# Kernel optimization log

Hardware: AMD Instinct MI355X
Metric: run time of the kernel (lower is better)

The kernel has to match this reference:

```python
import jax, jax.numpy as jnp
import numpy as np

N_NODES = 100000
N_EDGES = 500000
D = 128


def setup_inputs() -> dict:
    key = jax.random.key(0)
    ks = jax.random.split(key, 6)
    x = jax.random.normal(ks[0], (N_NODES, D), dtype=jnp.float32)
    edge_index = jax.random.randint(ks[1], (2, N_EDGES), 0, N_NODES, dtype=jnp.int64)
    edge_label = jax.random.randint(ks[2], (N_EDGES,), 0, 2, dtype=jnp.int64)
    # MLP params (dim_in -> dim_in, 2 layers, has_act=True, has_bias=True)
    scale = 1.0 / np.sqrt(D)
    W1 = jax.random.normal(ks[3], (D, D), dtype=jnp.float32) * scale
    b1 = jnp.zeros((D,), dtype=jnp.float32)
    W2 = jax.random.normal(ks[4], (D, D), dtype=jnp.float32) * scale
    b2 = jnp.zeros((D,), dtype=jnp.float32)
    return {"x": x, "edge_index": edge_index, "edge_label": edge_label,
            "W1": W1, "b1": b1, "W2": W2, "b2": b2}


def reference(x, edge_index, edge_label, W1, b1, W2, b2):
    # post-MP MLP on all node features (has_act=True -> ReLU after each layer)
    h = jax.nn.relu(x @ W1 + b1)          # [N, D]
    h = jax.nn.relu(h @ W2 + b2)          # [N, D]
    # gather endpoints: batch.x[edge_index] -> [2, E, D]
    v1 = h[edge_index[0]]                  # [E, D]
    v2 = h[edge_index[1]]                  # [E, D]
    # dot decode: sum(v1 * v2, dim=-1)
    pred = jnp.sum(v1 * v2, axis=-1)       # [E]
    return pred, edge_label
```

## Files before the change

### kernel.cpp

```cpp
#include <hip/hip_runtime.h>

typedef __attribute__((ext_vector_type(8))) short short8;
typedef __attribute__((ext_vector_type(4))) short short4v;
typedef __attribute__((ext_vector_type(4))) float floatx4;

#define D 128
#define NWAVES 4
#define GRID_MLP 512

__device__ __forceinline__ unsigned short f2bf(float f) {
  unsigned u = __float_as_uint(f);
  u += 0x7FFFu + ((u >> 16) & 1u);
  return (unsigned short)(u >> 16);
}

__device__ __forceinline__ void stageW(const float* __restrict__ W,
                                       unsigned short* __restrict__ sW, int tid) {
  const int n = tid & 127;
  const int tg = tid >> 7;
  #pragma unroll
  for (int iter = 0; iter < 16; ++iter) {
    const int k0 = iter * 8 + tg * 4;
    float w0 = W[(k0 + 0) * D + n];
    float w1 = W[(k0 + 1) * D + n];
    float w2 = W[(k0 + 2) * D + n];
    float w3 = W[(k0 + 3) * D + n];
    short4v p;
    p[0] = (short)f2bf(w0); p[1] = (short)f2bf(w1);
    p[2] = (short)f2bf(w2); p[3] = (short)f2bf(w3);
    const int idx = n * D + (((k0 >> 3) ^ (n & 15)) << 3) + (k0 & 7);
    *(short4v*)&sW[idx] = p;
  }
}

__device__ __forceinline__ short8 cvt_a(const floatx4& f0, const floatx4& f1) {
  short8 a;
  a[0] = (short)f2bf(f0[0]); a[1] = (short)f2bf(f0[1]);
  a[2] = (short)f2bf(f0[2]); a[3] = (short)f2bf(f0[3]);
  a[4] = (short)f2bf(f1[0]); a[5] = (short)f2bf(f1[1]);
  a[6] = (short)f2bf(f1[2]); a[7] = (short)f2bf(f1[3]);
  return a;
}

__global__ __launch_bounds__(256) void mlp_fused(
    const float* __restrict__ x, const float* __restrict__ W1,
    const float* __restrict__ b1, const float* __restrict__ W2,
    const float* __restrict__ b2, unsigned short* __restrict__ h,
    const int* __restrict__ elabel, float* __restrict__ out,
    int nNodes, int npairs, int E) {
  __shared__ unsigned short sW1[D * D];
  __shared__ unsigned short sW2[D * D];
  __shared__ unsigned short sH[NWAVES][16 * D];
  const int tid = threadIdx.x;
  const int wave = tid >> 6, lane = tid & 63;
  const int quad = lane >> 4, l16 = lane & 15;

  {
    const int E4 = E & ~3;
    for (int li = (blockIdx.x * 256 + tid) * 4; li < E4; li += GRID_MLP * 256 * 4) {
      int4 lv = *(const int4*)&elabel[li];
      float4 fv = make_float4((float)lv.x, (float)lv.y, (float)lv.z, (float)lv.w);
      *(float4*)&out[E + li] = fv;
    }
    if (blockIdx.x == 0 && tid < (E & 3)) out[E + E4 + tid] = (float)elabel[E4 + tid];
  }

  stageW(W1, sW1, tid);
  stageW(W2, sW2, tid);
  __syncthreads();

  float bias1[8], bias2[8];
  #pragma unroll
  for (int n0 = 0; n0 < 8; ++n0) { bias1[n0] = b1[n0 * 16 + l16]; bias2[n0] = b2[n0 * 16 + l16]; }

  unsigned short* mysH = sH[wave];

  for (int p = blockIdx.x * NWAVES + wave; p < npairs; p += GRID_MLP * NWAVES) {
    const int mbase = p * 32;
    const int m0 = mbase + l16;
    const int m1 = m0 + 16;
    floatx4 xf0[8], xf1[8];
    {
      const floatx4* xp0 = (const floatx4*)(x + (size_t)m0 * D + quad * 8);
      const floatx4* xp1 = (const floatx4*)(x + (size_t)m1 * D + quad * 8);
      const bool v0 = (m0 < nNodes), v1 = (m1 < nNodes);
      #pragma unroll
      for (int i = 0; i < 8; ++i) {
        const int o = (i >> 1) * 8 + (i & 1);
        xf0[i] = v0 ? xp0[o] : (floatx4){0.f, 0.f, 0.f, 0.f};
        xf1[i] = v1 ? xp1[o] : (floatx4){0.f, 0.f, 0.f, 0.f};
      }
    }
    floatx4 acc0[8], acc1[8];
    #pragma unroll
    for (int n0 = 0; n0 < 8; ++n0) {
      acc0[n0] = (floatx4){0.f, 0.f, 0.f, 0.f};
      acc1[n0] = (floatx4){0.f, 0.f, 0.f, 0.f};
    }
    #pragma unroll
    for (int kk = 0; kk < 4; ++kk) {
      const short8 a0 = cvt_a(xf0[2 * kk], xf0[2 * kk + 1]);
      const short8 a1 = cvt_a(xf1[2 * kk], xf1[2 * kk + 1]);
      #pragma unroll
      for (int n0 = 0; n0 < 8; ++n0) {
        short8 b = *(const short8*)&sW1[(n0 * 16 + l16) * D + (((kk * 4 + quad) ^ l16) << 3)];
        acc0[n0] = __builtin_amdgcn_mfma_f32_16x16x32_bf16(a0, b, acc0[n0], 0, 0, 0);
        acc1[n0] = __builtin_amdgcn_mfma_f32_16x16x32_bf16(a1, b, acc1[n0], 0, 0, 0);
      }
    }
    short8 af0[4], af1[4];
    #pragma unroll
    for (int n0 = 0; n0 < 8; ++n0) {
      #pragma unroll
      for (int r = 0; r < 4; ++r) {
        float v = acc0[n0][r] + bias1[n0];
        v = v > 0.f ? v : 0.f;
        const int row = quad * 4 + r;
        const int g = 2 * n0 + (l16 >> 3);
        mysH[row * D + (((g ^ row) & 15) << 3) + (l16 & 7)] = f2bf(v);
      }
    }
    #pragma unroll
    for (int kk = 0; kk < 4; ++kk)
      af0[kk] = *(const short8*)&mysH[l16 * D + ((((kk * 4 + quad) ^ l16) & 15) << 3)];
    #pragma unroll
    for (int n0 = 0; n0 < 8; ++n0) {
      #pragma unroll
      for (int r = 0; r < 4; ++r) {
        float v = acc1[n0][r] + bias1[n0];
        v = v > 0.f ? v : 0.f;
        const int row = quad * 4 + r;
        const int g = 2 * n0 + (l16 >> 3);
        mysH[row * D + (((g ^ row) & 15) << 3) + (l16 & 7)] = f2bf(v);
      }
    }
    #pragma unroll
    for (int kk = 0; kk < 4; ++kk)
      af1[kk] = *(const short8*)&mysH[l16 * D + ((((kk * 4 + quad) ^ l16) & 15) << 3)];
    #pragma unroll
    for (int n0 = 0; n0 < 8; ++n0) {
      acc0[n0] = (floatx4){0.f, 0.f, 0.f, 0.f};
      acc1[n0] = (floatx4){0.f, 0.f, 0.f, 0.f};
    }
    #pragma unroll
    for (int kk = 0; kk < 4; ++kk) {
      #pragma unroll
      for (int n0 = 0; n0 < 8; ++n0) {
        short8 b = *(const short8*)&sW2[(n0 * 16 + l16) * D + (((kk * 4 + quad) ^ l16) << 3)];
        acc0[n0] = __builtin_amdgcn_mfma_f32_16x16x32_bf16(af0[kk], b, acc0[n0], 0, 0, 0);
        acc1[n0] = __builtin_amdgcn_mfma_f32_16x16x32_bf16(af1[kk], b, acc1[n0], 0, 0, 0);
      }
    }
    #pragma unroll
    for (int n0 = 0; n0 < 8; ++n0) {
      #pragma unroll
      for (int r = 0; r < 4; ++r) {
        float v = acc0[n0][r] + bias2[n0];
        v = v > 0.f ? v : 0.f;
        const int row = quad * 4 + r;
        const int g = 2 * n0 + (l16 >> 3);
        mysH[row * D + (((g ^ row) & 15) << 3) + (l16 & 7)] = f2bf(v);
      }
    }
    #pragma unroll
    for (int i = 0; i < 4; ++i) {
      const int row = i * 4 + quad;
      short8 vrow = *(const short8*)&mysH[row * D + (((l16 ^ row) & 15) << 3)];
      const int g = mbase + row;
      if (g < nNodes) *(short8*)&h[(size_t)g * D + l16 * 8] = vrow;
    }
    #pragma unroll
    for (int n0 = 0; n0 < 8; ++n0) {
      #pragma unroll
      for (int r = 0; r < 4; ++r) {
        float v = acc1[n0][r] + bias2[n0];
        v = v > 0.f ? v : 0.f;
        const int row = quad * 4 + r;
        const int g = 2 * n0 + (l16 >> 3);
        mysH[row * D + (((g ^ row) & 15) << 3) + (l16 & 7)] = f2bf(v);
      }
    }
    #pragma unroll
    for (int i = 0; i < 4; ++i) {
      const int row = i * 4 + quad;
      short8 vrow = *(const short8*)&mysH[row * D + (((l16 ^ row) & 15) << 3)];
      const int g = mbase + 16 + row;
      if (g < nNodes) *(short8*)&h[(size_t)g * D + l16 * 8] = vrow;
    }
  }
}

__device__ __forceinline__ float dot2bf(unsigned a, unsigned b, float acc) {
  float a0 = __uint_as_float(a << 16);
  float a1 = __uint_as_float(a & 0xFFFF0000u);
  float b0 = __uint_as_float(b << 16);
  float b1 = __uint_as_float(b & 0xFFFF0000u);
  acc = fmaf(a0, b0, acc);
  acc = fmaf(a1, b1, acc);
  return acc;
}

__device__ __forceinline__ float edge_dot(const uint4& a, const uint4& b) {
  float acc = 0.f;
  acc = dot2bf(a.x, b.x, acc);
  acc = dot2bf(a.y, b.y, acc);
  acc = dot2bf(a.z, b.z, acc);
  acc = dot2bf(a.w, b.w, acc);
  acc += __shfl_xor(acc, 8);
  acc += __shfl_xor(acc, 4);
  acc += __shfl_xor(acc, 2);
  acc += __shfl_xor(acc, 1);
  return acc;
}

__global__ __launch_bounds__(256) void edge_kernel(
    const unsigned short* __restrict__ h2, const int* __restrict__ eidx,
    float* __restrict__ out, int E) {
  const int sub = threadIdx.x & 15;
  const int grp = (blockIdx.x * 256 + threadIdx.x) >> 4;
  const int e0 = grp * 8;
  if (e0 + 8 <= E) {
    const int4 s0 = *(const int4*)&eidx[e0];
    const int4 s1 = *(const int4*)&eidx[e0 + 4];
    const int4 t0 = *(const int4*)&eidx[E + e0];
    const int4 t1 = *(const int4*)&eidx[E + e0 + 4];
    int s[8] = {s0.x, s0.y, s0.z, s0.w, s1.x, s1.y, s1.z, s1.w};
    int d[8] = {t0.x, t0.y, t0.z, t0.w, t1.x, t1.y, t1.z, t1.w};
    uint4 va[8], vb[8];
    #pragma unroll
    for (int i = 0; i < 8; ++i) {
      va[i] = *(const uint4*)(h2 + (((size_t)(unsigned)s[i]) << 7) + sub * 8);
      vb[i] = *(const uint4*)(h2 + (((size_t)(unsigned)d[i]) << 7) + sub * 8);
    }
    #pragma unroll
    for (int i = 0; i < 8; ++i) {
      float acc = edge_dot(va[i], vb[i]);
      if (sub == 0) out[e0 + i] = acc;
    }
  } else if (e0 < E) {
    for (int e = e0; e < E; ++e) {
      const int s = eidx[e];
      const int d = eidx[E + e];
      const uint4 ua = *(const uint4*)(h2 + (((size_t)(unsigned)s) << 7) + sub * 8);
      const uint4 ub = *(const uint4*)(h2 + (((size_t)(unsigned)d) << 7) + sub * 8);
      float acc = edge_dot(ua, ub);
      if (sub == 0) out[e] = acc;
    }
  }
}

extern "C" void kernel_launch(void* const* d_in, const int* in_sizes, int n_in,
                              void* d_out, int out_size, void* d_ws, size_t ws_size,
                              hipStream_t stream) {
  const float* x  = (const float*)d_in[0];
  const int* eidx = (const int*)d_in[1];
  const int* elab = (const int*)d_in[2];
  const float* W1 = (const float*)d_in[3];
  const float* b1 = (const float*)d_in[4];
  const float* W2 = (const float*)d_in[5];
  const float* b2 = (const float*)d_in[6];
  float* out = (float*)d_out;

  const int nNodes = in_sizes[0] / D;
  const int E = in_sizes[2];
  const int npairs = (nNodes + 31) / 32;

  unsigned short* h = (unsigned short*)d_ws;

  mlp_fused<<<GRID_MLP, 256, 0, stream>>>(x, W1, b1, W2, b2, h, elab, out,
                                          nNodes, npairs, E);

  const int edgeBlocks = (E + 127) / 128;
  edge_kernel<<<edgeBlocks, 256, 0, stream>>>(h, eidx, out, E);
}
```

Baseline: 142.2 us.

## Pre-pack bf16 weights in MFMA fragment order in global memory and drop LDS staging

Adds a small prep kernel that converts W1/W2 to bf16 once per call and stores them in a global buffer already laid out in per-lane MFMA B-fragment order. The MLP kernel no longer stages the 64 KB of weights into LDS; each lane loads its B fragments straight from global/L2. The persistent 512-block grid-stride loop becomes one 32-row pair per wave with a grid sized to the node count. This cuts LDS use so more blocks fit per CU and removes the per-block weight staging and barrier. In exchange it adds an extra launch and repeated weight fragment reads from cache on every tile.

```diff
diff --git a/kernel.cpp b/kernel.cpp
--- a/kernel.cpp
+++ b/kernel.cpp
@@ -1,12 +1,12 @@
 #include <hip/hip_runtime.h>
 
 typedef __attribute__((ext_vector_type(8))) short short8;
-typedef __attribute__((ext_vector_type(4))) short short4v;
 typedef __attribute__((ext_vector_type(4))) float floatx4;
 
 #define D 128
 #define NWAVES 4
-#define GRID_MLP 512
+
+__device__ unsigned short g_wq[2 * D * D];
 
 __device__ __forceinline__ unsigned short f2bf(float f) {
   unsigned u = __float_as_uint(f);
@@ -14,23 +14,19 @@
   return (unsigned short)(u >> 16);
 }
 
-__device__ __forceinline__ void stageW(const float* __restrict__ W,
-                                       unsigned short* __restrict__ sW, int tid) {
-  const int n = tid & 127;
-  const int tg = tid >> 7;
-  #pragma unroll
-  for (int iter = 0; iter < 16; ++iter) {
-    const int k0 = iter * 8 + tg * 4;
-    float w0 = W[(k0 + 0) * D + n];
-    float w1 = W[(k0 + 1) * D + n];
-    float w2 = W[(k0 + 2) * D + n];
-    float w3 = W[(k0 + 3) * D + n];
-    short4v p;
-    p[0] = (short)f2bf(w0); p[1] = (short)f2bf(w1);
-    p[2] = (short)f2bf(w2); p[3] = (short)f2bf(w3);
-    const int idx = n * D + (((k0 >> 3) ^ (n & 15)) << 3) + (k0 & 7);
-    *(short4v*)&sW[idx] = p;
-  }
+__global__ __launch_bounds__(256) void prep_w(const float* __restrict__ W1,
+                                              const float* __restrict__ W2) {
+  const int t = blockIdx.x * 256 + threadIdx.x;
+  const int layer = t >> 14;
+  const int r = t & 16383;
+  const int fragid = r >> 9;
+  const int lane = (r >> 3) & 63;
+  const int e = r & 7;
+  const int kk = fragid >> 3, n0 = fragid & 7;
+  const int k = kk * 32 + (lane >> 4) * 8 + e;
+  const int n = n0 * 16 + (lane & 15);
+  const float* W = layer ? W2 : W1;
+  g_wq[t] = f2bf(W[k * D + n]);
 }
 
 __device__ __forceinline__ short8 cvt_a(const floatx4& f0, const floatx4& f1) {
@@ -42,14 +38,11 @@
   return a;
 }
 
-__global__ __launch_bounds__(256) void mlp_fused(
-    const float* __restrict__ x, const float* __restrict__ W1,
-    const float* __restrict__ b1, const float* __restrict__ W2,
-    const float* __restrict__ b2, unsigned short* __restrict__ h,
-    const int* __restrict__ elabel, float* __restrict__ out,
-    int nNodes, int npairs, int E) {
-  __shared__ unsigned short sW1[D * D];
-  __shared__ unsigned short sW2[D * D];
+__global__ __launch_bounds__(256, 4) void mlp_fused(
+    const float* __restrict__ x,
+    const float* __restrict__ b1, const float* __restrict__ b2,
+    unsigned short* __restrict__ h, const int* __restrict__ elabel,
+    float* __restrict__ out, int nNodes, int npairs, int E) {
   __shared__ unsigned short sH[NWAVES][16 * D];
   const int tid = threadIdx.x;
   const int wave = tid >> 6, lane = tid & 63;
@@ -57,7 +50,7 @@
 
   {
     const int E4 = E & ~3;
-    for (int li = (blockIdx.x * 256 + tid) * 4; li < E4; li += GRID_MLP * 256 * 4) {
+    for (int li = (blockIdx.x * 256 + tid) * 4; li < E4; li += gridDim.x * 256 * 4) {
       int4 lv = *(const int4*)&elabel[li];
       float4 fv = make_float4((float)lv.x, (float)lv.y, (float)lv.z, (float)lv.w);
       *(float4*)&out[E + li] = fv;
@@ -65,128 +58,127 @@
     if (blockIdx.x == 0 && tid < (E & 3)) out[E + E4 + tid] = (float)elabel[E4 + tid];
   }
 
-  stageW(W1, sW1, tid);
-  stageW(W2, sW2, tid);
-  __syncthreads();
+  const int p = blockIdx.x * NWAVES + wave;
+  if (p >= npairs) return;
 
   float bias1[8], bias2[8];
   #pragma unroll
   for (int n0 = 0; n0 < 8; ++n0) { bias1[n0] = b1[n0 * 16 + l16]; bias2[n0] = b2[n0 * 16 + l16]; }
 
+  const short8* wq1 = (const short8*)g_wq;
+  const short8* wq2 = (const short8*)(g_wq + 16384);
   unsigned short* mysH = sH[wave];
 
-  for (int p = blockIdx.x * NWAVES + wave; p < npairs; p += GRID_MLP * NWAVES) {
-    const int mbase = p * 32;
-    const int m0 = mbase + l16;
-    const int m1 = m0 + 16;
-    floatx4 xf0[8], xf1[8];
-    {
-      const floatx4* xp0 = (const floatx4*)(x + (size_t)m0 * D + quad * 8);
-      const floatx4* xp1 = (const floatx4*)(x + (size_t)m1 * D + quad * 8);
-      const bool v0 = (m0 < nNodes), v1 = (m1 < nNodes);
-      #pragma unroll
-      for (int i = 0; i < 8; ++i) {
-        const int o = (i >> 1) * 8 + (i & 1);
-        xf0[i] = v0 ? xp0[o] : (floatx4){0.f, 0.f, 0.f, 0.f};
-        xf1[i] = v1 ? xp1[o] : (floatx4){0.f, 0.f, 0.f, 0.f};
-      }
-    }
-    floatx4 acc0[8], acc1[8];
+  const int mbase = p * 32;
+  const int m0 = mbase + l16;
+  const int m1 = m0 + 16;
+  floatx4 xf0[8], xf1[8];
+  {
+    const floatx4* xp0 = (const floatx4*)(x + (size_t)m0 * D + quad * 8);
+    const floatx4* xp1 = (const floatx4*)(x + (size_t)m1 * D + quad * 8);
+    const bool v0 = (m0 < nNodes), v1 = (m1 < nNodes);
+    #pragma unroll
+    for (int i = 0; i < 8; ++i) {
+      const int o = (i >> 1) * 8 + (i & 1);
+      xf0[i] = v0 ? xp0[o] : (floatx4){0.f, 0.f, 0.f, 0.f};
+      xf1[i] = v1 ? xp1[o] : (floatx4){0.f, 0.f, 0.f, 0.f};
+    }
+  }
+  floatx4 acc0[8], acc1[8];
+  #pragma unroll
+  for (int n0 = 0; n0 < 8; ++n0) {
+    acc0[n0] = (floatx4){0.f, 0.f, 0.f, 0.f};
+    acc1[n0] = (floatx4){0.f, 0.f, 0.f, 0.f};
+  }
+  #pragma unroll
+  for (int kk = 0; kk < 4; ++kk) {
+    const short8 a0 = cvt_a(xf0[2 * kk], xf0[2 * kk + 1]);
+    const short8 a1 = cvt_a(xf1[2 * kk], xf1[2 * kk + 1]);
     #pragma unroll
     for (int n0 = 0; n0 < 8; ++n0) {
-      acc0[n0] = (floatx4){0.f, 0.f, 0.f, 0.f};
-      acc1[n0] = (floatx4){0.f, 0.f, 0.f, 0.f};
-    }
-    #pragma unroll
-    for (int kk = 0; kk < 4; ++kk) {
-      const short8 a0 = cvt_a(xf0[2 * kk], xf0[2 * kk + 1]);
-      const short8 a1 = cvt_a(xf1[2 * kk], xf1[2 * kk + 1]);
-      #pragma unroll
-      for (int n0 = 0; n0 < 8; ++n0) {
-        short8 b = *(const short8*)&sW1[(n0 * 16 + l16) * D + (((kk * 4 + quad) ^ l16) << 3)];
-        acc0[n0] = __builtin_amdgcn_mfma_f32_16x16x32_bf16(a0, b, acc0[n0], 0, 0, 0);
-        acc1[n0] = __builtin_amdgcn_mfma_f32_16x16x32_bf16(a1, b, acc1[n0], 0, 0, 0);
-      }
-    }
-    short8 af0[4], af1[4];
+      short8 b = wq1[(kk * 8 + n0) * 64 + lane];
+      acc0[n0] = __builtin_amdgcn_mfma_f32_16x16x32_bf16(a0, b, acc0[n0], 0, 0, 0);
+      acc1[n0] = __builtin_amdgcn_mfma_f32_16x16x32_bf16(a1, b, acc1[n0], 0, 0, 0);
+    }
+  }
+  short8 af0[4], af1[4];
+  #pragma unroll
+  for (int n0 = 0; n0 < 8; ++n0) {
+    #pragma unroll
+    for (int r = 0; r < 4; ++r) {
+      float v = acc0[n0][r] + bias1[n0];
+      v = v > 0.f ? v : 0.f;
+      const int row = quad * 4 + r;
+      const int g = 2 * n0 + (l16 >> 3);
+      mysH[row * D + (((g ^ row) & 15) << 3) + (l16 & 7)] = f2bf(v);
+    }
+  }
+  #pragma unroll
+  for (int kk = 0; kk < 4; ++kk)
+    af0[kk] = *(const short8*)&mysH[l16 * D + ((((kk * 4 + quad) ^ l16) & 15) << 3)];
+  #pragma unroll
+  for (int n0 = 0; n0 < 8; ++n0) {
+    #pragma unroll
+    for (int r = 0; r < 4; ++r) {
+      float v = acc1[n0][r] + bias1[n0];
+      v = v > 0.f ? v : 0.f;
+      const int row = quad * 4 + r;
+      const int g = 2 * n0 + (l16 >> 3);
+      mysH[row * D + (((g ^ row) & 15) << 3) + (l16 & 7)] = f2bf(v);
+    }
+  }
+  #pragma unroll
+  for (int kk = 0; kk < 4; ++kk)
+    af1[kk] = *(const short8*)&mysH[l16 * D + ((((kk * 4 + quad) ^ l16) & 15) << 3)];
+  #pragma unroll
+  for (int n0 = 0; n0 < 8; ++n0) {
+    acc0[n0] = (floatx4){0.f, 0.f, 0.f, 0.f};
+    acc1[n0] = (floatx4){0.f, 0.f, 0.f, 0.f};
+  }
+  #pragma unroll
+  for (int kk = 0; kk < 4; ++kk) {
     #pragma unroll
     for (int n0 = 0; n0 < 8; ++n0) {
-      #pragma unroll
-      for (int r = 0; r < 4; ++r) {
-        float v = acc0[n0][r] + bias1[n0];
-        v = v > 0.f ? v : 0.f;
-        const int row = quad * 4 + r;
-        const int g = 2 * n0 + (l16 >> 3);
-        mysH[row * D + (((g ^ row) & 15) << 3) + (l16 & 7)] = f2bf(v);
-      }
-    }
-    #pragma unroll
-    for (int kk = 0; kk < 4; ++kk)
-      af0[kk] = *(const short8*)&mysH[l16 * D + ((((kk * 4 + quad) ^ l16) & 15) << 3)];
-    #pragma unroll
-    for (int n0 = 0; n0 < 8; ++n0) {
-      #pragma unroll
-      for (int r = 0; r < 4; ++r) {
-        float v = acc1[n0][r] + bias1[n0];
-        v = v > 0.f ? v : 0.f;
-        const int row = quad * 4 + r;
-        const int g = 2 * n0 + (l16 >> 3);
-        mysH[row * D + (((g ^ row) & 15) << 3) + (l16 & 7)] = f2bf(v);
-      }
-    }
-    #pragma unroll
-    for (int kk = 0; kk < 4; ++kk)
-      af1[kk] = *(const short8*)&mysH[l16 * D + ((((kk * 4 + quad) ^ l16) & 15) << 3)];
-    #pragma unroll
-    for (int n0 = 0; n0 < 8; ++n0) {
-      acc0[n0] = (floatx4){0.f, 0.f, 0.f, 0.f};
-      acc1[n0] = (floatx4){0.f, 0.f, 0.f, 0.f};
-    }
-    #pragma unroll
-    for (int kk = 0; kk < 4; ++kk) {
-      #pragma unroll
-      for (int n0 = 0; n0 < 8; ++n0) {
-        short8 b = *(const short8*)&sW2[(n0 * 16 + l16) * D + (((kk * 4 + quad) ^ l16) << 3)];
-        acc0[n0] = __builtin_amdgcn_mfma_f32_16x16x32_bf16(af0[kk], b, acc0[n0], 0, 0, 0);
-        acc1[n0] = __builtin_amdgcn_mfma_f32_16x16x32_bf16(af1[kk], b, acc1[n0], 0, 0, 0);
-      }
-    }
-    #pragma unroll
-    for (int n0 = 0; n0 < 8; ++n0) {
-      #pragma unroll
-      for (int r = 0; r < 4; ++r) {
-        float v = acc0[n0][r] + bias2[n0];
-        v = v > 0.f ? v : 0.f;
-        const int row = quad * 4 + r;
-        const int g = 2 * n0 + (l16 >> 3);
-        mysH[row * D + (((g ^ row) & 15) << 3) + (l16 & 7)] = f2bf(v);
-      }
-    }
-    #pragma unroll
-    for (int i = 0; i < 4; ++i) {
-      const int row = i * 4 + quad;
-      short8 vrow = *(const short8*)&mysH[row * D + (((l16 ^ row) & 15) << 3)];
-      const int g = mbase + row;
-      if (g < nNodes) *(short8*)&h[(size_t)g * D + l16 * 8] = vrow;
-    }
-    #pragma unroll
-    for (int n0 = 0; n0 < 8; ++n0) {
-      #pragma unroll
-      for (int r = 0; r < 4; ++r) {
-        float v = acc1[n0][r] + bias2[n0];
-        v = v > 0.f ? v : 0.f;
-        const int row = quad * 4 + r;
-        const int g = 2 * n0 + (l16 >> 3);
-        mysH[row * D + (((g ^ row) & 15) << 3) + (l16 & 7)] = f2bf(v);
-      }
-    }
-    #pragma unroll
-    for (int i = 0; i < 4; ++i) {
-      const int row = i * 4 + quad;
-      short8 vrow = *(const short8*)&mysH[row * D + (((l16 ^ row) & 15) << 3)];
-      const int g = mbase + 16 + row;
-      if (g < nNodes) *(short8*)&h[(size_t)g * D + l16 * 8] = vrow;
-    }
+      short8 b = wq2[(kk * 8 + n0) * 64 + lane];
+      acc0[n0] = __builtin_amdgcn_mfma_f32_16x16x32_bf16(af0[kk], b, acc0[n0], 0, 0, 0);
+      acc1[n0] = __builtin_amdgcn_mfma_f32_16x16x32_bf16(af1[kk], b, acc1[n0], 0, 0, 0);
+    }
+  }
+  #pragma unroll
+  for (int n0 = 0; n0 < 8; ++n0) {
+    #pragma unroll
+    for (int r = 0; r < 4; ++r) {
+      float v = acc0[n0][r] + bias2[n0];
+      v = v > 0.f ? v : 0.f;
+      const int row = quad * 4 + r;
+      const int g = 2 * n0 + (l16 >> 3);
+      mysH[row * D + (((g ^ row) & 15) << 3) + (l16 & 7)] = f2bf(v);
+    }
+  }
+  #pragma unroll
+  for (int i = 0; i < 4; ++i) {
+    const int row = i * 4 + quad;
+    short8 vrow = *(const short8*)&mysH[row * D + (((l16 ^ row) & 15) << 3)];
+    const int g = mbase + row;
+    if (g < nNodes) *(short8*)&h[(size_t)g * D + l16 * 8] = vrow;
+  }
+  #pragma unroll
+  for (int n0 = 0; n0 < 8; ++n0) {
+    #pragma unroll
+    for (int r = 0; r < 4; ++r) {
+      float v = acc1[n0][r] + bias2[n0];
+      v = v > 0.f ? v : 0.f;
+      const int row = quad * 4 + r;
+      const int g = 2 * n0 + (l16 >> 3);
+      mysH[row * D + (((g ^ row) & 15) << 3) + (l16 & 7)] = f2bf(v);
+    }
+  }
+  #pragma unroll
+  for (int i = 0; i < 4; ++i) {
+    const int row = i * 4 + quad;
+    short8 vrow = *(const short8*)&mysH[row * D + (((l16 ^ row) & 15) << 3)];
+    const int g = mbase + 16 + row;
+    if (g < nNodes) *(short8*)&h[(size_t)g * D + l16 * 8] = vrow;
   }
 }
 
@@ -267,8 +259,10 @@
 
   unsigned short* h = (unsigned short*)d_ws;
 
-  mlp_fused<<<GRID_MLP, 256, 0, stream>>>(x, W1, b1, W2, b2, h, elab, out,
-                                          nNodes, npairs, E);
+  prep_w<<<128, 256, 0, stream>>>(W1, W2);
+
+  const int nblk = (npairs + NWAVES - 1) / NWAVES;
+  mlp_fused<<<nblk, 256, 0, stream>>>(x, b1, b2, h, elab, out, nNodes, npairs, E);
 
   const int edgeBlocks = (E + 127) / 128;
   edge_kernel<<<edgeBlocks, 256, 0, stream>>>(h, eidx, out, E);
```

New measurement: 164.0 us. +15.3%, slower.
